# Kernel tuning notes

Hardware: AMD Instinct MI355X
Metric: run time of the kernel (lower is better)

## Reference

```python
import jax, jax.numpy as jnp
import numpy as np

INNER_DIM = 256
DT_SIZE = 64
STATE_DIM = 256  # must equal INNER_DIM for the original split() to be valid
BATCH, SEQ_LEN = 2, 512


def setup_inputs() -> dict:
    key = jax.random.key(0)
    k_x, k_win, k_wdt, k_bdt = jax.random.split(key, 4)
    x = jax.random.normal(k_x, (BATCH, SEQ_LEN, INNER_DIM), dtype=jnp.float32)
    # nn.Linear(inner_dim, dt_size + 2*state_dim, bias=False); stored as [in, out] for x @ W
    W_in = jax.random.normal(k_win, (INNER_DIM, DT_SIZE + 2 * STATE_DIM), dtype=jnp.float32) / np.sqrt(INNER_DIM)
    # nn.Linear(dt_size, inner_dim) with bias
    W_dt = jax.random.normal(k_wdt, (DT_SIZE, INNER_DIM), dtype=jnp.float32) / np.sqrt(DT_SIZE)
    b_dt = jax.random.normal(k_bdt, (INNER_DIM,), dtype=jnp.float32) * 0.01
    # alpha_log = log(repeat(arange(1, N+1), 'n -> d n'))
    alpha_log = jnp.log(jnp.broadcast_to(
        jnp.arange(1, STATE_DIM + 1, dtype=jnp.float32), (INNER_DIM, STATE_DIM)))
    delta = jnp.ones((INNER_DIM,), dtype=jnp.float32)
    return {"input_tensor": x, "W_in": W_in, "W_dt": W_dt, "b_dt": b_dt,
            "alpha_log": alpha_log, "delta": delta}


def reference(input_tensor, W_in, W_dt, b_dt, alpha_log, delta):
    x = input_tensor
    alpha = -jnp.exp(alpha_log)  # [D, N]
    proj = x @ W_in  # [B, L, DT + 2D]
    dt_raw, beta, gamma = jnp.split(proj, [DT_SIZE, DT_SIZE + INNER_DIM], axis=-1)
    dt = jax.nn.softplus(dt_raw @ W_dt + b_dt)  # [B, L, D]
    # dt_a = exp(dt[...,None] * alpha) : [B, L, D, N]
    dt_a = jnp.exp(jnp.einsum('bld,dn->bldn', dt, alpha))
    # dt_b_i = dt * x outer beta : [B, L, D, N]
    dt_b_i = jnp.einsum('bld,bln->bldn', dt * x, beta)

    def step(state, inputs):
        a_t, b_t, g_t = inputs  # [B,D,N], [B,D,N], [B,N]
        state = a_t * state + b_t
        y_t = jnp.einsum('bdn,bn->bd', state, g_t)
        return state, y_t

    s0 = jnp.zeros((x.shape[0], INNER_DIM, STATE_DIM), dtype=x.dtype)
    _, ys = jax.lax.scan(step, s0, (jnp.moveaxis(dt_a, 1, 0),
                                    jnp.moveaxis(dt_b_i, 1, 0),
                                    jnp.moveaxis(gamma, 1, 0)))
    ys = jnp.moveaxis(ys, 0, 1)  # [B, L, D]
    return ys + x * delta
```

## Files before the change

### kernel.cpp

```cpp
#include <hip/hip_runtime.h>
#include <math.h>

#define DIM   256
#define NST   256
#define LSEQ  512
#define BAT   2
#define DTSZ  64
#define PCOLS 576
#define NROWS 1024

typedef float    f32x4 __attribute__((ext_vector_type(4)));
typedef unsigned u32x4 __attribute__((ext_vector_type(4)));

constexpr float LOG2E = 1.4426950408889634f;

__device__ __forceinline__ float fexp2(float v) {
#if __has_builtin(__builtin_amdgcn_exp2f)
    return __builtin_amdgcn_exp2f(v);
#else
    return exp2f(v);
#endif
}

__device__ __forceinline__ float softplusf(float v) {
    return (v > 20.f) ? v : log1pf(__expf(v));
}

__device__ __forceinline__ void barrier_lds_only() {
    __builtin_amdgcn_s_waitcnt(0xC07F);
    __builtin_amdgcn_s_barrier();
}

__device__ __forceinline__ unsigned pack_bg(float be, float ga) {
    unsigned ub = __float_as_uint(be);
    unsigned ug = __float_as_uint(ga);
    ub = (ub + 0x7fffu + ((ub >> 16) & 1u)) >> 16;
    ug = (ug + 0x7fffu + ((ug >> 16) & 1u)) & 0xffff0000u;
    return ub | ug;
}

__device__ __forceinline__ unsigned short rne16(float f) {
    unsigned u = __float_as_uint(f);
    return (unsigned short)((u + 0x7fffu + ((u >> 16) & 1u)) >> 16);
}

__device__ __forceinline__ unsigned cvtpk(float lo, float hi) {
    unsigned r;
    asm("v_cvt_pk_bf16_f32 %0, %1, %2" : "=v"(r) : "v"(lo), "v"(hi));
    return r;
}

__device__ __forceinline__ f32x4 mfma16(u32x4 a, u32x4 b, f32x4 c) {
    asm("v_mfma_f32_16x16x32_bf16 %0, %1, %2, %0" : "+v"(c) : "v"(a), "v"(b));
    return c;
}

__global__ __launch_bounds__(256) void proj_mfma(
    const float* __restrict__ x, const float* __restrict__ W_in,
    unsigned* __restrict__ betgam,
    float* __restrict__ draw)
{
    __shared__ unsigned short Bt[64][264];
    const int tid  = threadIdx.x;
    const int lane = tid & 63;
    const int mt   = blockIdx.x / 9;
    const int role = blockIdx.x % 9;

    const int base0 = (role < 8) ? (64  + 32 * role) : 0;
    const int base1 = (role < 8) ? (320 + 32 * role) : 32;
    {
        const int cl = tid & 31;
        const int kq = tid >> 5;
        #pragma unroll 8
        for (int p = 0; p < 32; ++p) {
            const int k = p * 8 + kq;
            const float v0 = W_in[k * PCOLS + base0 + cl];
            const float v1 = W_in[k * PCOLS + base1 + cl];
            Bt[cl][k]      = rne16(v0);
            Bt[32 + cl][k] = rne16(v1);
        }
    }
    __syncthreads();

    const int w    = tid >> 6;
    const int wm   = w >> 1, wn = w & 1;
    const int row  = mt * 32 + wm * 16 + (lane & 15);
    const int koff = (lane >> 4) * 8;
    const float* xp = x + row * DIM + koff;
    const unsigned short* bp1 = &Bt[16 * wn + (lane & 15)][koff];
    const unsigned short* bp2 = &Bt[32 + 16 * wn + (lane & 15)][koff];

    f32x4 acc1 = {0.f, 0.f, 0.f, 0.f};
    f32x4 acc2 = {0.f, 0.f, 0.f, 0.f};
    #pragma unroll
    for (int kk = 0; kk < 8; ++kk) {
        const float4 xa = *(const float4*)(xp + kk * 32);
        const float4 xb = *(const float4*)(xp + kk * 32 + 4);
        u32x4 a;
        a.x = cvtpk(xa.x, xa.y);
        a.y = cvtpk(xa.z, xa.w);
        a.z = cvtpk(xb.x, xb.y);
        a.w = cvtpk(xb.z, xb.w);
        const u32x4 b1 = *(const u32x4*)(bp1 + kk * 32);
        const u32x4 b2 = *(const u32x4*)(bp2 + kk * 32);
        acc1 = mfma16(a, b1, acc1);
        acc2 = mfma16(a, b2, acc2);
    }

    const int rowbase = mt * 32 + wm * 16 + (lane >> 4) * 4;
    if (role < 8) {
        const int n = 32 * role + 16 * wn + (lane & 15);
        #pragma unroll
        for (int r = 0; r < 4; ++r)
            betgam[(rowbase + r) * NST + n] = pack_bg(acc1[r], acc2[r]);
    } else {
        const int c1 = 16 * wn + (lane & 15);
        #pragma unroll
        for (int r = 0; r < 4; ++r) {
            draw[(rowbase + r) * DTSZ + c1]      = acc1[r];
            draw[(rowbase + r) * DTSZ + 32 + c1] = acc2[r];
        }
    }
}

__global__ __launch_bounds__(256, 2) void scan1p(
    const float* __restrict__ x,
    const float* __restrict__ alpha_log,
    const float* __restrict__ delta,
    const unsigned* __restrict__ betgam,
    const float* __restrict__ draw,
    const float* __restrict__ W_dt,
    const float* __restrict__ b_dt,
    float* __restrict__ out)
{
    __shared__ float part[32][NST];
    __shared__ float dts[LSEQ], dxs[LSEQ], xcol[LSEQ];
    __shared__ float wdt[DTSZ];
    const int n = threadIdx.x;
    const int xcd  = blockIdx.x & 7;
    const int slot = blockIdx.x >> 3;
    const int b = xcd >> 2;
    const int d = slot * 4 + (xcd & 3);
    const int rb = b * LSEQ;

    if (n < DTSZ) wdt[n] = W_dt[n * DIM + d];
    #pragma unroll
    for (int it = 0; it < 2; ++it) {
        const int l = n + it * 256;
        xcol[l] = x[(rb + l) * DIM + d];
    }
    const float aln = -__expf(alpha_log[d * NST + n]) * LOG2E;
    const float dv  = delta[d];
    const float bdv = b_dt[d];
    __syncthreads();

    #pragma unroll
    for (int it = 0; it < 2; ++it) {
        const int l = n + it * 256;
        const float4* dr = (const float4*)&draw[(rb + l) * DTSZ];
        float acc = bdv;
        #pragma unroll
        for (int c = 0; c < 16; ++c) {
            const float4 v  = dr[c];
            const float4 wv = *(const float4*)&wdt[c * 4];
            acc = fmaf(v.x, wv.x, acc);
            acc = fmaf(v.y, wv.y, acc);
            acc = fmaf(v.z, wv.z, acc);
            acc = fmaf(v.w, wv.w, acc);
        }
        const float sp = softplusf(acc);
        dts[l] = sp;
        dxs[l] = sp * xcol[l];
    }
    __syncthreads();

    float s = 0.f;
    unsigned bg[8][8];
    #pragma unroll
    for (int pw = 0; pw < 6; ++pw) {
        #pragma unroll
        for (int t = 0; t < 8; ++t)
            bg[pw][t] = betgam[(rb + pw * 8 + t) * NST + n];
    }

    #pragma unroll 8
    for (int w = 0; w < 64; ++w) {
        const int cur = w & 7;
        const int pf  = (w + 6) & 7;
        if (w + 6 < 64) {
            #pragma unroll
            for (int t = 0; t < 8; ++t)
                bg[pf][t] = betgam[(rb + (w + 6) * 8 + t) * NST + n];
        }
        float4 dta = *(const float4*)&dts[w * 8];
        float4 dtb = *(const float4*)&dts[w * 8 + 4];
        float4 dxa = *(const float4*)&dxs[w * 8];
        float4 dxb = *(const float4*)&dxs[w * 8 + 4];
        const float dtw[8] = {dta.x, dta.y, dta.z, dta.w, dtb.x, dtb.y, dtb.z, dtb.w};
        const float dxw[8] = {dxa.x, dxa.y, dxa.z, dxa.w, dxb.x, dxb.y, dxb.z, dxb.w};

        const int prow = (w & 3) * 8;
        #pragma unroll
        for (int t = 0; t < 8; ++t) {
            const unsigned u = bg[cur][t];
            const float be = __uint_as_float(u << 16);
            const float ga = __uint_as_float(u & 0xffff0000u);
            float a = fexp2(dtw[t] * aln);
            s = fmaf(a, s, dxw[t] * be);
            part[prow + t][n] = s * ga;
        }

        if ((w & 3) == 3) {
            barrier_lds_only();
            const int trow = n >> 3, seg = n & 7;
            float sum = 0.f;
            #pragma unroll
            for (int k = 0; k < 32; ++k)
                sum += part[trow][seg * 32 + ((k + n) & 31)];
            sum += __shfl_xor(sum, 1);
            sum += __shfl_xor(sum, 2);
            sum += __shfl_xor(sum, 4);
            if (seg == 0) {
                const int l = (w >> 2) * 32 + trow;
                out[(rb + l) * DIM + d] = sum + xcol[l] * dv;
            }
            barrier_lds_only();
        }
    }
}

extern "C" void kernel_launch(void* const* d_in, const int* in_sizes, int n_in,
                              void* d_out, int out_size, void* d_ws, size_t ws_size,
                              hipStream_t stream) {
    const float* x         = (const float*)d_in[0];
    const float* W_in      = (const float*)d_in[1];
    const float* W_dt      = (const float*)d_in[2];
    const float* b_dt      = (const float*)d_in[3];
    const float* alpha_log = (const float*)d_in[4];
    const float* delta     = (const float*)d_in[5];
    float* out = (float*)d_out;

    unsigned* betgam = (unsigned*)d_ws;
    float* draw = (float*)(betgam + NROWS * NST);

    proj_mfma<<<32 * 9, 256, 0, stream>>>(x, W_in, betgam, draw);
    scan1p<<<BAT * DIM, 256, 0, stream>>>(x, alpha_log, delta, betgam,
                                          draw, W_dt, b_dt, out);
}
```

Baseline: 111.3 us.

## Interleave beta/gamma buffer as 4-row vectors and issue scan prefetch earlier

```diff
diff --git a/kernel.cpp b/kernel.cpp
--- a/kernel.cpp
+++ b/kernel.cpp
@@ -55,9 +55,9 @@
     return c;
 }
 
-__global__ __launch_bounds__(256) void proj_mfma(
+__global__ __launch_bounds__(256, 2) void proj_mfma(
     const float* __restrict__ x, const float* __restrict__ W_in,
-    unsigned* __restrict__ betgam,
+    u32x4* __restrict__ betgam4,
     float* __restrict__ draw)
 {
     __shared__ unsigned short Bt[64][264];
@@ -74,10 +74,8 @@
         #pragma unroll 8
         for (int p = 0; p < 32; ++p) {
             const int k = p * 8 + kq;
-            const float v0 = W_in[k * PCOLS + base0 + cl];
-            const float v1 = W_in[k * PCOLS + base1 + cl];
-            Bt[cl][k]      = rne16(v0);
-            Bt[32 + cl][k] = rne16(v1);
+            Bt[cl][k]      = rne16(W_in[k * PCOLS + base0 + cl]);
+            Bt[32 + cl][k] = rne16(W_in[k * PCOLS + base1 + cl]);
         }
     }
     __syncthreads();
@@ -110,9 +108,12 @@
     const int rowbase = mt * 32 + wm * 16 + (lane >> 4) * 4;
     if (role < 8) {
         const int n = 32 * role + 16 * wn + (lane & 15);
-        #pragma unroll
-        for (int r = 0; r < 4; ++r)
-            betgam[(rowbase + r) * NST + n] = pack_bg(acc1[r], acc2[r]);
+        u32x4 st;
+        st.x = pack_bg(acc1[0], acc2[0]);
+        st.y = pack_bg(acc1[1], acc2[1]);
+        st.z = pack_bg(acc1[2], acc2[2]);
+        st.w = pack_bg(acc1[3], acc2[3]);
+        betgam4[(rowbase >> 2) * NST + n] = st;
     } else {
         const int c1 = 16 * wn + (lane & 15);
         #pragma unroll
@@ -127,7 +128,7 @@
     const float* __restrict__ x,
     const float* __restrict__ alpha_log,
     const float* __restrict__ delta,
-    const unsigned* __restrict__ betgam,
+    const u32x4* __restrict__ betgam4,
     const float* __restrict__ draw,
     const float* __restrict__ W_dt,
     const float* __restrict__ b_dt,
@@ -141,7 +142,8 @@
     const int slot = blockIdx.x >> 3;
     const int b = xcd >> 2;
     const int d = slot * 4 + (xcd & 3);
-    const int rb = b * LSEQ;
+    const int rb  = b * LSEQ;
+    const int rbq = rb >> 2;
 
     if (n < DTSZ) wdt[n] = W_dt[n * DIM + d];
     #pragma unroll
@@ -152,7 +154,16 @@
     const float aln = -__expf(alpha_log[d * NST + n]) * LOG2E;
     const float dv  = delta[d];
     const float bdv = b_dt[d];
-    __syncthreads();
+
+    u32x4 bg[8][2];
+    #pragma unroll
+    for (int pw = 0; pw < 6; ++pw) {
+        #pragma unroll
+        for (int h = 0; h < 2; ++h)
+            bg[pw][h] = betgam4[(rbq + pw * 2 + h) * NST + n];
+    }
+
+    barrier_lds_only();
 
     #pragma unroll
     for (int it = 0; it < 2; ++it) {
@@ -175,22 +186,13 @@
     __syncthreads();
 
     float s = 0.f;
-    unsigned bg[8][8];
-    #pragma unroll
-    for (int pw = 0; pw < 6; ++pw) {
-        #pragma unroll
-        for (int t = 0; t < 8; ++t)
-            bg[pw][t] = betgam[(rb + pw * 8 + t) * NST + n];
-    }
-
     #pragma unroll 8
     for (int w = 0; w < 64; ++w) {
         const int cur = w & 7;
         const int pf  = (w + 6) & 7;
         if (w + 6 < 64) {
-            #pragma unroll
-            for (int t = 0; t < 8; ++t)
-                bg[pf][t] = betgam[(rb + (w + 6) * 8 + t) * NST + n];
+            bg[pf][0] = betgam4[(rbq + (w + 6) * 2)     * NST + n];
+            bg[pf][1] = betgam4[(rbq + (w + 6) * 2 + 1) * NST + n];
         }
         float4 dta = *(const float4*)&dts[w * 8];
         float4 dtb = *(const float4*)&dts[w * 8 + 4];
@@ -202,7 +204,7 @@
         const int prow = (w & 3) * 8;
         #pragma unroll
         for (int t = 0; t < 8; ++t) {
-            const unsigned u = bg[cur][t];
+            const unsigned u = bg[cur][t >> 2][t & 3];
             const float be = __uint_as_float(u << 16);
             const float ga = __uint_as_float(u & 0xffff0000u);
             float a = fexp2(dtw[t] * aln);
@@ -240,10 +242,10 @@
     const float* delta     = (const float*)d_in[5];
     float* out = (float*)d_out;
 
-    unsigned* betgam = (unsigned*)d_ws;
-    float* draw = (float*)(betgam + NROWS * NST);
-
-    proj_mfma<<<32 * 9, 256, 0, stream>>>(x, W_in, betgam, draw);
-    scan1p<<<BAT * DIM, 256, 0, stream>>>(x, alpha_log, delta, betgam,
+    u32x4* betgam4 = (u32x4*)d_ws;
+    float* draw    = (float*)(betgam4 + (NROWS / 4) * NST);
+
+    proj_mfma<<<32 * 9, 256, 0, stream>>>(x, W_in, betgam4, draw);
+    scan1p<<<BAT * DIM, 256, 0, stream>>>(x, alpha_log, delta, betgam4,
                                           draw, W_dt, b_dt, out);
 }
```

New measurement: 107.1 us. 1.04x faster.
